# Performance work log

Measured on AMD Instinct MI355X. Metric: run time of the kernel, lower is better.

## Reference

```python
import jax, jax.numpy as jnp
import numpy as np
from jax import lax

B = 4096          # graphs in batch
NPG = 50          # nodes per graph
N = B * NPG       # 204800 nodes
E = N * 8         # 1638400 directed edges
F_IN = 128
H = 64            # GCN hidden
K = 10            # SortPooling k
NUM_CLASSES = 10


def _glorot(key, shape):
    lim = float(np.sqrt(6.0 / (shape[0] + shape[1])))
    return jax.random.uniform(key, shape, jnp.float32, -lim, lim)


def setup_inputs() -> dict:
    key = jax.random.key(0)
    ks = jax.random.split(key, 10)
    x = jax.random.normal(ks[0], (N, F_IN), jnp.float32)
    edge_index = jax.random.randint(ks[1], (2, E), 0, N)
    batch = jnp.repeat(jnp.arange(B), NPG)  # sorted graph ids, 50 nodes each
    return {
        "x": x, "edge_index": edge_index, "batch": batch,
        "W1": _glorot(ks[2], (F_IN, H)), "b1": jnp.zeros((H,), jnp.float32),
        "W2": _glorot(ks[3], (H, H)), "b2": jnp.zeros((H,), jnp.float32),
        "W3": _glorot(ks[4], (H, H)), "b3": jnp.zeros((H,), jnp.float32),
        "Wc1": jax.random.normal(ks[5], (32, K, 4), jnp.float32) * 0.05,
        "bc1": jnp.zeros((32,), jnp.float32),
        "Wc2": jax.random.normal(ks[6], (64, 32, 3), jnp.float32) * 0.05,
        "bc2": jnp.zeros((64,), jnp.float32),
        "Wf": _glorot(ks[7], (H, NUM_CLASSES)),
        "bf": jnp.zeros((NUM_CLASSES,), jnp.float32),
    }


def reference(x, edge_index, batch, W1, b1, W2, b2, W3, b3, Wc1, bc1, Wc2, bc2, Wf, bf):
    row, col = edge_index[0], edge_index[1]
    # PyG GCNConv normalization with self-loops: deg over targets + 1
    deg = jax.ops.segment_sum(jnp.ones((E,), jnp.float32), col, num_segments=N) + 1.0
    dinv = lax.rsqrt(deg)
    ecoef = (dinv[row] * dinv[col])[:, None]   # [E,1] edge norm
    scoef = (dinv * dinv)[:, None]             # [N,1] self-loop norm

    def gcn(h, W, b):
        h = h @ W
        agg = jax.ops.segment_sum(h[row] * ecoef, col, num_segments=N) + h * scoef
        return agg + b

    x1 = jnp.tanh(gcn(x, W1, b1))
    x2 = jnp.tanh(gcn(x1, W2, b2))
    x3 = jnp.tanh(gcn(x2, W3, b3))
    feat = jnp.concatenate([x1, x2, x3], axis=-1)   # JK cat -> [N, 192]

    # DGL SortPooling(k=10): sort each node's features ascending, then take
    # top-k nodes per graph by the last (largest) feature, descending.
    feat = jnp.sort(feat, axis=-1)
    order = jnp.lexsort((-feat[:, -1], batch))      # graph asc, key desc
    fs, bs = feat[order], batch[order]
    counts = jax.ops.segment_sum(jnp.ones((N,), jnp.int32), batch, num_segments=B)
    starts = jnp.cumsum(counts) - counts
    rank = jnp.arange(N) - starts[bs]               # within-graph rank
    mask = (rank < K)[:, None]
    pooled = jnp.zeros((B, K, feat.shape[-1]), feat.dtype)
    pooled = pooled.at[bs, jnp.minimum(rank, K - 1)].add(jnp.where(mask, fs, 0.0))

    h = pooled  # [B, 10, 192] == x.view(B, 10, 192)
    h = lax.conv_general_dilated(h, Wc1, (4,), 'VALID',
                                 dimension_numbers=('NCH', 'OIH', 'NCH')) + bc1[None, :, None]
    h = jax.nn.relu(h)                              # [B,32,48]
    h = lax.reduce_window(h, -jnp.inf, lax.max, (1, 1, 4), (1, 1, 4), 'VALID')  # [B,32,12]
    h = lax.conv_general_dilated(h, Wc2, (3,), 'VALID',
                                 dimension_numbers=('NCH', 'OIH', 'NCH')) + bc2[None, :, None]
    h = jax.nn.relu(h)                              # [B,64,4]
    h = lax.reduce_window(h, -jnp.inf, lax.max, (1, 1, 4), (1, 1, 4), 'VALID')  # [B,64,1]
    xf = h.reshape(B, -1)                           # [B,64]
    c = jax.nn.relu(xf) @ Wf + bf                   # [B,num_classes]
    return (c, xf)
```

## Files before the change

### kernel.cpp

```cpp
#include <hip/hip_runtime.h>
#include <hip/hip_bf16.h>

#define NN 204800
#define EE 1638400
#define BBATCH 4096
#define NPGRAPH 50
#define KTOP 10
#define NBLK 200

#define OFF_W1  0
#define OFF_W2  8192
#define OFF_W3  12288
#define OFF_B1  16384
#define OFF_B2  16448
#define OFF_B3  16512
#define OFF_WC1 16576
#define OFF_BC1 17856
#define OFF_WC2 17888
#define OFF_BC2 24032
#define OFF_WF  24096
#define OFF_BF  24736
#define WTOT    24746

__device__ __forceinline__ float bf2f(unsigned short u) {
    unsigned int x = ((unsigned int)u) << 16;
    float f; __builtin_memcpy(&f, &x, 4); return f;
}

__device__ __forceinline__ long long pack_sc(int s, float c) {
    return ((long long)(unsigned)__float_as_int(c) << 32) | (unsigned)s;
}

__global__ void detect_kernel(const unsigned int* __restrict__ xw,
                              const unsigned int* __restrict__ eiw,
                              int* __restrict__ flags) {
    __shared__ int s_f32, s_i64;
    int t = threadIdx.x;
    if (t == 0) { s_f32 = 0; s_i64 = 1; }
    __syncthreads();
    unsigned w = xw[t];
    unsigned u0 = w & 0xffffu, u1 = w >> 16;
    int e0 = (u0 >> 7) & 0xff, e1 = (u1 >> 7) & 0xff;
    if (e0 >= 0x88 || e1 >= 0x88) atomicOr(&s_f32, 1);
    if (eiw[2 * t + 1] != 0) atomicAnd(&s_i64, 0);
    __syncthreads();
    if (t == 0) { flags[0] = s_f32; flags[1] = s_i64; }
}


struct WPtrs { const void* p[12]; };

__global__ void convert_weights_kernel(WPtrs wp, const int* __restrict__ flags,
                                       float* __restrict__ dst) {
    const int lens[12] = {8192,4096,4096,64,64,64,1280,32,6144,64,640,10};
    const int offs[12] = {OFF_W1,OFF_W2,OFF_W3,OFF_B1,OFF_B2,OFF_B3,
                          OFF_WC1,OFF_BC1,OFF_WC2,OFF_BC2,OFF_WF,OFF_BF};
    int f32 = flags[0];
    int t = blockIdx.x * 256 + threadIdx.x;
    for (int s = 0; s < 12; ++s) {
        if (t < lens[s]) {
            float v = f32 ? ((const float*)wp.p[s])[t]
                          : bf2f(((const unsigned short*)wp.p[s])[t]);
            dst[offs[s] + t] = v;
            return;
        }
        t -= lens[s];
    }
}


__global__ void zero_int_kernel(int* p, int n) {
    int i = blockIdx.x * 256 + threadIdx.x;
    if (i < n) p[i] = 0;
}

__device__ __forceinline__ int ld_idx(const void* ei, int i64, long pos) {
    return i64 ? (int)((const long long*)ei)[pos] : ((const int*)ei)[pos];
}

__global__ void count_kernel(const void* __restrict__ ei, const int* __restrict__ flags,
                             int* __restrict__ cnt) {
    int e = blockIdx.x * 256 + threadIdx.x;
    if (e >= EE) return;
    int c = ld_idx(ei, flags[1], (long)EE + e);
    atomicAdd(&cnt[c], 1);
}

__global__ __launch_bounds__(1024) void scan1_kernel(const int* __restrict__ cnt,
                                                     int* __restrict__ offs,
                                                     float* __restrict__ dinv,
                                                     int* __restrict__ blksum) {
    __shared__ int wsum[16];
    int b = blockIdx.x, t = threadIdx.x;
    int lane = t & 63, wid = t >> 6;
    int i = b * 1024 + t;
    int v = cnt[i] + 1;
    int x = v;
    #pragma unroll
    for (int d = 1; d < 64; d <<= 1) { int y = __shfl_up(x, d, 64); if (lane >= d) x += y; }
    if (lane == 63) wsum[wid] = x;
    __syncthreads();
    if (t == 0) {
        int run = 0;
        #pragma unroll
        for (int k = 0; k < 16; ++k) { int tmp = wsum[k]; wsum[k] = run; run += tmp; }
        blksum[b] = run;
    }
    __syncthreads();
    offs[i] = wsum[wid] + x - v;
    dinv[i] = (float)(1.0 / sqrt((double)v));
}

__global__ __launch_bounds__(256) void scan2_kernel(int* __restrict__ blksum) {
    __shared__ int wsum[4];
    int t = threadIdx.x, lane = t & 63, wid = t >> 6;
    int v = (t < NBLK) ? blksum[t] : 0;
    int x = v;
    #pragma unroll
    for (int d = 1; d < 64; d <<= 1) { int y = __shfl_up(x, d, 64); if (lane >= d) x += y; }
    if (lane == 63) wsum[wid] = x;
    __syncthreads();
    int pre = 0;
    for (int k = 0; k < wid; ++k) pre += wsum[k];
    if (t < NBLK) blksum[t] = pre + x - v;
}

__global__ __launch_bounds__(1024) void scan3_kernel(int* __restrict__ offs,
                                                     const int* __restrict__ blksum) {
    int b = blockIdx.x, i = b * 1024 + threadIdx.x;
    offs[i] += blksum[b];
    if (i == 0) offs[NN] = EE + NN;
}

__global__ void fill_self_kernel(const int* __restrict__ offs, const float* __restrict__ dinv,
                                 int* __restrict__ cursor, long long* __restrict__ epack) {
    int n = blockIdx.x * 256 + threadIdx.x;
    if (n >= NN) return;
    int p = offs[n];
    float d = dinv[n];
    __builtin_nontemporal_store(pack_sc(n, d * d), &epack[p]);
    cursor[n] = 1;
}

__global__ void fill_edges_kernel(const void* __restrict__ ei, const int* __restrict__ flags,
                                  const int* __restrict__ offs,
                                  const float* __restrict__ dinv, int* __restrict__ cursor,
                                  long long* __restrict__ epack) {
    int e = blockIdx.x * 256 + threadIdx.x;
    if (e >= EE) return;
    int i64 = flags[1];
    int r = ld_idx(ei, i64, e);
    int c = ld_idx(ei, i64, (long)EE + e);
    int p = offs[c] + atomicAdd(&cursor[c], 1);
    __builtin_nontemporal_store(pack_sc(r, dinv[r] * dinv[c]), &epack[p]);
}


template<int KD, int MODE>
__global__ __launch_bounds__(256) void xw_kernel(const void* __restrict__ xin_,
                                                 const int* __restrict__ flags,
                                                 int row_stride, int col_off,
                                                 const float* __restrict__ W,
                                                 float* __restrict__ hout) {
    constexpr int CH = 32;
    __shared__ float xs[256 * 36];
    int t = threadIdx.x;
    long row0 = (long)blockIdx.x * 256;
    bool bf16in = (MODE == 1) && (flags[0] == 0);
    float acc[64];
    #pragma unroll
    for (int c = 0; c < 64; ++c) acc[c] = 0.f;

    for (int kb = 0; kb < KD; kb += CH) {
        __syncthreads();
        if (bf16in) {
            const unsigned short* x = (const unsigned short*)xin_;
            unsigned short* xsh = (unsigned short*)xs;
            #pragma unroll
            for (int rr = 0; rr < 32; ++rr) {
                int idx = rr * 256 + t;
                int r = idx >> 5, k = idx & 31;
                xsh[r * 40 + k] = x[(row0 + r) * row_stride + col_off + kb + k];
            }
        } else {
            const float* x = (const float*)xin_;
            #pragma unroll
            for (int rr = 0; rr < 32; ++rr) {
                int idx = rr * 256 + t;
                int r = idx >> 5, k = idx & 31;
                xs[r * 36 + k] = x[(row0 + r) * row_stride + col_off + kb + k];
            }
        }
        __syncthreads();
        if (bf16in) {
            #pragma unroll 2
            for (int k = 0; k < CH; ++k) {
                float xk = bf2f(((unsigned short*)xs)[t * 40 + k]);
                const float* wr = W + (kb + k) * 64;
                #pragma unroll
                for (int c = 0; c < 64; ++c) acc[c] = fmaf(xk, wr[c], acc[c]);
            }
        } else {
            #pragma unroll 2
            for (int k = 0; k < CH; ++k) {
                float xk = xs[t * 36 + k];
                const float* wr = W + (kb + k) * 64;
                #pragma unroll
                for (int c = 0; c < 64; ++c) acc[c] = fmaf(xk, wr[c], acc[c]);
            }
        }
    }
    float* o = hout + (row0 + t) * 64;
    #pragma unroll
    for (int c = 0; c < 64; c += 4) {
        float4 v; v.x = acc[c]; v.y = acc[c+1]; v.z = acc[c+2]; v.w = acc[c+3];
        *(float4*)(o + c) = v;
    }
}


__global__ __launch_bounds__(256) void spmm_kernel(const float* __restrict__ h,
                                                   const int* __restrict__ offs,
                                                   const long long* __restrict__ epack,
                                                   const float* __restrict__ bias,
                                                   float* __restrict__ featOut,
                                                   float* __restrict__ keyOut) {
    int node = blockIdx.x * 4 + (threadIdx.x >> 6);
    int lane = threadIdx.x & 63;
    int j0 = offs[node], j1 = offs[node + 1];
    float acc = 0.f;

    for (int base = j0; base < j1; base += 64) {
        int n = j1 - base; if (n > 64) n = 64;
        long long my = 0;
        if (lane < n) my = epack[base + lane];

        int m = 0;
        for (; m + 8 <= n; m += 8) {
            float hv[8], cf[8];
            #pragma unroll
            for (int u = 0; u < 8; ++u) {
                long long e = __shfl(my, m + u, 64);
                int s = (int)(unsigned)e;
                cf[u] = __int_as_float((int)(e >> 32));
                hv[u] = h[(long)s * 64 + lane];
            }
            #pragma unroll
            for (int u = 0; u < 8; ++u) acc = fmaf(hv[u], cf[u], acc);
        }
        for (; m < n; ++m) {
            long long e = __shfl(my, m, 64);
            int s = (int)(unsigned)e;
            float cf = __int_as_float((int)(e >> 32));
            acc = fmaf(h[(long)s * 64 + lane], cf, acc);
        }
    }

    float val = tanhf(acc + bias[lane]);
    featOut[(long)node * 192 + lane] = val;
    float m = val;
    #pragma unroll
    for (int d = 32; d; d >>= 1) m = fmaxf(m, __shfl_xor(m, d, 64));
    if (lane == 0) keyOut[node] = m;
}


__global__ __launch_bounds__(256) void select_topk_kernel(const float* __restrict__ key3,
                                                          int* __restrict__ topidx) {
    int g = blockIdx.x * 4 + (threadIdx.x >> 6);
    int lane = threadIdx.x & 63;
    int node = g * NPGRAPH + lane;
    float k = -INFINITY;
    if (lane < NPGRAPH)
        k = fmaxf(fmaxf(key3[node], key3[NN + node]), key3[2 * NN + node]);
    for (int r = 0; r < KTOP; ++r) {
        float bk = k; int bi = lane;
        #pragma unroll
        for (int d = 32; d; d >>= 1) {
            float ok = __shfl_xor(bk, d, 64);
            int   oi = __shfl_xor(bi, d, 64);
            if (ok > bk || (ok == bk && oi < bi)) { bk = ok; bi = oi; }
        }
        if (lane == 0) topidx[g * KTOP + r] = g * NPGRAPH + bi;
        if (lane == bi) k = -INFINITY;
    }
}


__global__ __launch_bounds__(256) void sort_gather_kernel(const float* __restrict__ feat,
                                                          const int* __restrict__ topidx,
                                                          float* __restrict__ pooled) {
    int lane = threadIdx.x & 63;
    int w = threadIdx.x >> 6;
    int slot = blockIdx.x * 4 + w;
    int node = topidx[slot];

    unsigned v[4];
    #pragma unroll
    for (int t = 0; t < 3; ++t) {
        float x = feat[(long)node * 192 + 64 * t + lane];
        unsigned u = __float_as_uint(x);
        v[t] = (u & 0x80000000u) ? ~u : (u | 0x80000000u);
    }
    v[3] = 0xFF800000u;

    #pragma unroll
    for (int k = 2; k <= 256; k <<= 1) {
        #pragma unroll
        for (int d = 128; d >= 1; d >>= 1) {
            if (d >= k) continue;
            if (d >= 64) {
                int dt = d >> 6;
                #pragma unroll
                for (int t = 0; t < 4; ++t) {
                    if (!(t & dt)) {
                        int t2 = t | dt;
                        bool asc = ((64 * t) & k) == 0;
                        unsigned a = v[t], b = v[t2];
                        unsigned mn = a < b ? a : b;
                        unsigned mx = a < b ? b : a;
                        v[t]  = asc ? mn : mx;
                        v[t2] = asc ? mx : mn;
                    }
                }
            } else {
                #pragma unroll
                for (int t = 0; t < 4; ++t) {
                    unsigned p = (unsigned)__shfl_xor((int)v[t], d, 64);
                    int e = 64 * t + lane;
                    bool lower = (lane & d) == 0;
                    bool asc = (e & k) == 0;
                    unsigned mn = v[t] < p ? v[t] : p;
                    unsigned mx = v[t] < p ? p : v[t];
                    v[t] = (lower == asc) ? mn : mx;
                }
            }
        }
    }

    #pragma unroll
    for (int t = 0; t < 3; ++t) {
        unsigned kk = v[t];
        unsigned u = (kk & 0x80000000u) ? (kk ^ 0x80000000u) : ~kk;
        pooled[(long)slot * 192 + 64 * t + lane] = __uint_as_float(u);
    }
}


__global__ __launch_bounds__(256) void conv1_kernel(const float* __restrict__ pooled,
                                                    const float* __restrict__ wc,
                                                    float* __restrict__ pool1) {
    __shared__ float p[1920];
    __shared__ float w[1280];
    __shared__ float c1[1536];
    int b = blockIdx.x, t = threadIdx.x;
    for (int i = t; i < 1920; i += 256) p[i] = pooled[(long)b * 1920 + i];
    for (int i = t; i < 1280; i += 256) w[i] = wc[OFF_WC1 + i];
    __syncthreads();
    for (int o = t; o < 1536; o += 256) {
        int oc = o / 48, s = o % 48;
        float acc = wc[OFF_BC1 + oc];
        #pragma unroll
        for (int ic = 0; ic < 10; ++ic)
            #pragma unroll
            for (int t4 = 0; t4 < 4; ++t4)
                acc = fmaf(p[ic * 192 + s * 4 + t4], w[oc * 40 + ic * 4 + t4], acc);
        c1[o] = fmaxf(acc, 0.f);
    }
    __syncthreads();
    for (int o = t; o < 384; o += 256) {
        int oc = o / 12, q = o % 12;
        float m = c1[oc * 48 + q * 4];
        #pragma unroll
        for (int u = 1; u < 4; ++u) m = fmaxf(m, c1[oc * 48 + q * 4 + u]);
        pool1[(long)b * 384 + o] = m;
    }
}


__global__ __launch_bounds__(256) void conv2_fc_kernel(const float* __restrict__ pool1,
                                                       const float* __restrict__ wc,
                                                       const int* __restrict__ flags,
                                                       void* __restrict__ outv) {
    __shared__ float p[384];
    __shared__ float w2[6144];
    __shared__ float r2[256];
    __shared__ float xfs[64];
    int b = blockIdx.x, t = threadIdx.x;
    int f32o = flags[0];
    for (int i = t; i < 384; i += 256) p[i] = pool1[(long)b * 384 + i];
    for (int i = t; i < 6144; i += 256) w2[i] = wc[OFF_WC2 + i];
    __syncthreads();
    {
        int oc = t >> 2, s = t & 3;
        float acc = wc[OFF_BC2 + oc];
        #pragma unroll
        for (int ic = 0; ic < 32; ++ic)
            #pragma unroll
            for (int t3 = 0; t3 < 3; ++t3)
                acc = fmaf(p[ic * 12 + 3 * s + t3], w2[oc * 96 + ic * 3 + t3], acc);
        r2[t] = fmaxf(acc, 0.f);
    }
    __syncthreads();
    if (t < 64) {
        float m = fmaxf(fmaxf(r2[4*t], r2[4*t+1]), fmaxf(r2[4*t+2], r2[4*t+3]));
        xfs[t] = m;
        long idx = (long)BBATCH * 10 + (long)b * 64 + t;
        if (f32o) ((float*)outv)[idx] = m;
        else      ((__hip_bfloat16*)outv)[idx] = __float2bfloat16(m);
    }
    __syncthreads();
    if (t < 10) {
        float acc = wc[OFF_BF + t];
        #pragma unroll
        for (int o = 0; o < 64; ++o)
            acc = fmaf(fmaxf(xfs[o], 0.f), wc[OFF_WF + o * 10 + t], acc);
        long idx = (long)b * 10 + t;
        if (f32o) ((float*)outv)[idx] = acc;
        else      ((__hip_bfloat16*)outv)[idx] = __float2bfloat16(acc);
    }
}


extern "C" void kernel_launch(void* const* d_in, const int* in_sizes, int n_in,
                              void* d_out, int out_size, void* d_ws, size_t ws_size,
                              hipStream_t stream) {
    const void* x  = d_in[0];
    const void* ei = d_in[1];
    WPtrs wp;
    wp.p[0] = d_in[3];
    wp.p[1] = d_in[5];
    wp.p[2] = d_in[7];
    wp.p[3] = d_in[4];
    wp.p[4] = d_in[6];
    wp.p[5] = d_in[8];
    wp.p[6] = d_in[9];
    wp.p[7] = d_in[10];
    wp.p[8] = d_in[11];
    wp.p[9] = d_in[12];
    wp.p[10] = d_in[13];
    wp.p[11] = d_in[14];

    char* ws = (char*)d_ws;
    size_t o = 0;
    auto take = [&](size_t bytes) { char* r = ws + o; o = (o + bytes + 255) & ~(size_t)255; return r; };
    int*       flags  = (int*)      take(2 * 4);
    float*     wconv  = (float*)    take((size_t)WTOT * 4);
    int*       offs   = (int*)      take((size_t)(NN + 1) * 4);
    long long* epack  = (long long*)take((size_t)(EE + NN) * 8);
    float*     key3   = (float*)    take((size_t)3 * NN * 4);
    int*       topidx = (int*)      take((size_t)BBATCH * KTOP * 4);
    int*       blksum = (int*)      take((size_t)NBLK * 4);
    char*      hbase  = take((size_t)NN * 64 * 4);
    float*     feat   = (float*)    take((size_t)NN * 192 * 4);

    float* h      = (float*)hbase;
    int*   cnt    = (int*)(hbase);
    int*   cursor = (int*)(hbase + (1u << 20));
    float* dinv   = (float*)(hbase + (2u << 20));
    float* pooled = (float*)(hbase);
    float* pool1  = (float*)(hbase + (34u << 20));

    detect_kernel<<<1, 256, 0, stream>>>((const unsigned int*)x, (const unsigned int*)ei, flags);
    convert_weights_kernel<<<(WTOT + 255) / 256, 256, 0, stream>>>(wp, flags, wconv);
    zero_int_kernel<<<NN / 256, 256, 0, stream>>>(cnt, NN);
    count_kernel<<<EE / 256, 256, 0, stream>>>(ei, flags, cnt);
    scan1_kernel<<<NBLK, 1024, 0, stream>>>(cnt, offs, dinv, blksum);
    scan2_kernel<<<1, 256, 0, stream>>>(blksum);
    scan3_kernel<<<NBLK, 1024, 0, stream>>>(offs, blksum);
    fill_self_kernel<<<NN / 256, 256, 0, stream>>>(offs, dinv, cursor, epack);
    fill_edges_kernel<<<EE / 256, 256, 0, stream>>>(ei, flags, offs, dinv, cursor, epack);

    xw_kernel<128, 1><<<NN / 256, 256, 0, stream>>>(x, flags, 128, 0, wconv + OFF_W1, h);
    spmm_kernel<<<NN / 4, 256, 0, stream>>>(h, offs, epack, wconv + OFF_B1, feat, key3);
    xw_kernel<64, 0><<<NN / 256, 256, 0, stream>>>(feat, flags, 192, 0, wconv + OFF_W2, h);
    spmm_kernel<<<NN / 4, 256, 0, stream>>>(h, offs, epack, wconv + OFF_B2, feat + 64, key3 + NN);
    xw_kernel<64, 0><<<NN / 256, 256, 0, stream>>>(feat, flags, 192, 64, wconv + OFF_W3, h);
    spmm_kernel<<<NN / 4, 256, 0, stream>>>(h, offs, epack, wconv + OFF_B3, feat + 128, key3 + 2 * NN);

    select_topk_kernel<<<BBATCH / 4, 256, 0, stream>>>(key3, topidx);
    sort_gather_kernel<<<BBATCH * KTOP / 4, 256, 0, stream>>>(feat, topidx, pooled);
    conv1_kernel<<<BBATCH, 256, 0, stream>>>(pooled, wconv, pool1);
    conv2_fc_kernel<<<BBATCH, 256, 0, stream>>>(pool1, wconv, flags, d_out);
}
```

Before: 978.8 us.

## Rewrite dense XW as lane-per-output-column with weights held in registers

```diff
diff --git a/kernel.cpp b/kernel.cpp
--- a/kernel.cpp
+++ b/kernel.cpp
@@ -20,7 +20,11 @@
 #define OFF_BC2 24032
 #define OFF_WF  24096
 #define OFF_BF  24736
-#define WTOT    24746
+#define WSUM    24746
+#define OFF_W1T 24748
+#define OFF_W2T 32944
+#define OFF_W3T 37044
+#define WTOT    41140
 
 __device__ __forceinline__ float bf2f(unsigned short u) {
     unsigned int x = ((unsigned int)u) << 16;
@@ -62,6 +66,9 @@
             float v = f32 ? ((const float*)wp.p[s])[t]
                           : bf2f(((const unsigned short*)wp.p[s])[t]);
             dst[offs[s] + t] = v;
+            if (s == 0)      dst[OFF_W1T + (t & 63) * 128 + (t >> 6)] = v;
+            else if (s == 1) dst[OFF_W2T + (t & 63) * 64 + (t >> 6)] = v;
+            else if (s == 2) dst[OFF_W3T + (t & 63) * 64 + (t >> 6)] = v;
             return;
         }
         t -= lens[s];
@@ -157,64 +164,72 @@
 
 
 template<int KD, int MODE>
-__global__ __launch_bounds__(256) void xw_kernel(const void* __restrict__ xin_,
-                                                 const int* __restrict__ flags,
-                                                 int row_stride, int col_off,
-                                                 const float* __restrict__ W,
-                                                 float* __restrict__ hout) {
-    constexpr int CH = 32;
-    __shared__ float xs[256 * 36];
-    int t = threadIdx.x;
-    long row0 = (long)blockIdx.x * 256;
+__global__ __launch_bounds__(256) void xw2_kernel(const void* __restrict__ xin_,
+                                                  const int* __restrict__ flags,
+                                                  int row_stride, int col_off,
+                                                  const float* __restrict__ WT,
+                                                  float* __restrict__ hout) {
+    int lane = threadIdx.x & 63;
+    int wid  = __builtin_amdgcn_readfirstlane(threadIdx.x >> 6);
     bool bf16in = (MODE == 1) && (flags[0] == 0);
-    float acc[64];
-    #pragma unroll
-    for (int c = 0; c < 64; ++c) acc[c] = 0.f;
-
-    for (int kb = 0; kb < KD; kb += CH) {
-        __syncthreads();
+
+    float wreg[KD];
+    {
+        const float4* wp4 = (const float4*)(WT + lane * KD);
+        #pragma unroll
+        for (int q = 0; q < KD / 4; ++q) {
+            float4 v = wp4[q];
+            wreg[4*q] = v.x; wreg[4*q+1] = v.y; wreg[4*q+2] = v.z; wreg[4*q+3] = v.w;
+        }
+    }
+
+    const int RPB = 128;
+    long rowBase = (long)blockIdx.x * RPB;
+    for (int it = 0; it < RPB / 16; ++it) {
+        long r0 = rowBase + it * 16 + wid * 4;
+        float acc[4] = {0.f, 0.f, 0.f, 0.f};
         if (bf16in) {
-            const unsigned short* x = (const unsigned short*)xin_;
-            unsigned short* xsh = (unsigned short*)xs;
             #pragma unroll
-            for (int rr = 0; rr < 32; ++rr) {
-                int idx = rr * 256 + t;
-                int r = idx >> 5, k = idx & 31;
-                xsh[r * 40 + k] = x[(row0 + r) * row_stride + col_off + kb + k];
+            for (int kc = 0; kc < KD; kc += 32) {
+                #pragma unroll
+                for (int i = 0; i < 4; ++i) {
+                    const uint4* xr = (const uint4*)((const unsigned short*)xin_
+                                        + (r0 + i) * row_stride + col_off + kc);
+                    #pragma unroll
+                    for (int q4 = 0; q4 < 4; ++q4) {
+                        uint4 raw = xr[q4];
+                        unsigned rw[4] = {raw.x, raw.y, raw.z, raw.w};
+                        #pragma unroll
+                        for (int q = 0; q < 4; ++q) {
+                            int k = kc + q4 * 8 + 2 * q;
+                            acc[i] = fmaf(__uint_as_float(rw[q] << 16),         wreg[k],     acc[i]);
+                            acc[i] = fmaf(__uint_as_float(rw[q] & 0xffff0000u), wreg[k + 1], acc[i]);
+                        }
+                    }
+                }
             }
         } else {
-            const float* x = (const float*)xin_;
             #pragma unroll
-            for (int rr = 0; rr < 32; ++rr) {
-                int idx = rr * 256 + t;
-                int r = idx >> 5, k = idx & 31;
-                xs[r * 36 + k] = x[(row0 + r) * row_stride + col_off + kb + k];
+            for (int kc = 0; kc < KD; kc += 16) {
+                #pragma unroll
+                for (int i = 0; i < 4; ++i) {
+                    const float4* xr = (const float4*)((const float*)xin_
+                                        + (r0 + i) * row_stride + col_off + kc);
+                    #pragma unroll
+                    for (int q4 = 0; q4 < 4; ++q4) {
+                        float4 v = xr[q4];
+                        int k = kc + 4 * q4;
+                        acc[i] = fmaf(v.x, wreg[k],     acc[i]);
+                        acc[i] = fmaf(v.y, wreg[k + 1], acc[i]);
+                        acc[i] = fmaf(v.z, wreg[k + 2], acc[i]);
+                        acc[i] = fmaf(v.w, wreg[k + 3], acc[i]);
+                    }
+                }
             }
         }
-        __syncthreads();
-        if (bf16in) {
-            #pragma unroll 2
-            for (int k = 0; k < CH; ++k) {
-                float xk = bf2f(((unsigned short*)xs)[t * 40 + k]);
-                const float* wr = W + (kb + k) * 64;
-                #pragma unroll
-                for (int c = 0; c < 64; ++c) acc[c] = fmaf(xk, wr[c], acc[c]);
-            }
-        } else {
-            #pragma unroll 2
-            for (int k = 0; k < CH; ++k) {
-                float xk = xs[t * 36 + k];
-                const float* wr = W + (kb + k) * 64;
-                #pragma unroll
-                for (int c = 0; c < 64; ++c) acc[c] = fmaf(xk, wr[c], acc[c]);
-            }
-        }
-    }
-    float* o = hout + (row0 + t) * 64;
-    #pragma unroll
-    for (int c = 0; c < 64; c += 4) {
-        float4 v; v.x = acc[c]; v.y = acc[c+1]; v.z = acc[c+2]; v.w = acc[c+3];
-        *(float4*)(o + c) = v;
+        #pragma unroll
+        for (int i = 0; i < 4; ++i)
+            hout[(r0 + i) * 64 + lane] = acc[i];
     }
 }
 
@@ -462,7 +477,7 @@
     float* pool1  = (float*)(hbase + (34u << 20));
 
     detect_kernel<<<1, 256, 0, stream>>>((const unsigned int*)x, (const unsigned int*)ei, flags);
-    convert_weights_kernel<<<(WTOT + 255) / 256, 256, 0, stream>>>(wp, flags, wconv);
+    convert_weights_kernel<<<(WSUM + 255) / 256, 256, 0, stream>>>(wp, flags, wconv);
     zero_int_kernel<<<NN / 256, 256, 0, stream>>>(cnt, NN);
     count_kernel<<<EE / 256, 256, 0, stream>>>(ei, flags, cnt);
     scan1_kernel<<<NBLK, 1024, 0, stream>>>(cnt, offs, dinv, blksum);
@@ -471,11 +486,11 @@
     fill_self_kernel<<<NN / 256, 256, 0, stream>>>(offs, dinv, cursor, epack);
     fill_edges_kernel<<<EE / 256, 256, 0, stream>>>(ei, flags, offs, dinv, cursor, epack);
 
-    xw_kernel<128, 1><<<NN / 256, 256, 0, stream>>>(x, flags, 128, 0, wconv + OFF_W1, h);
+    xw2_kernel<128, 1><<<NN / 128, 256, 0, stream>>>(x, flags, 128, 0, wconv + OFF_W1T, h);
     spmm_kernel<<<NN / 4, 256, 0, stream>>>(h, offs, epack, wconv + OFF_B1, feat, key3);
-    xw_kernel<64, 0><<<NN / 256, 256, 0, stream>>>(feat, flags, 192, 0, wconv + OFF_W2, h);
+    xw2_kernel<64, 0><<<NN / 128, 256, 0, stream>>>(feat, flags, 192, 0, wconv + OFF_W2T, h);
     spmm_kernel<<<NN / 4, 256, 0, stream>>>(h, offs, epack, wconv + OFF_B2, feat + 64, key3 + NN);
-    xw_kernel<64, 0><<<NN / 256, 256, 0, stream>>>(feat, flags, 192, 64, wconv + OFF_W3, h);
+    xw2_kernel<64, 0><<<NN / 128, 256, 0, stream>>>(feat, flags, 192, 64, wconv + OFF_W3T, h);
     spmm_kernel<<<NN / 4, 256, 0, stream>>>(h, offs, epack, wconv + OFF_B3, feat + 128, key3 + 2 * NN);
 
     select_topk_kernel<<<BBATCH / 4, 256, 0, stream>>>(key3, topidx);
```

New measurement: 1.567 ms. +60.1%, slower.
